# Optimization experiments

Measured on AMD Instinct MI355X. Metric: run time of the kernel, lower is better.

Reference implementation:

```python
import jax, jax.numpy as jnp
import numpy as np

B, N, S, K, D = 16, 4096, 1024, 32, 64
MLP = (64, 64, 128)
EPS = 1e-5  # BatchNorm2d default eps


def setup_inputs() -> dict:
    key = jax.random.key(0)
    ks = jax.random.split(key, 16)
    inp = {
        'xyz': jax.random.normal(ks[0], (B, N, 3), dtype=jnp.float32),
        'normals': jax.random.normal(ks[1], (B, N, 3), dtype=jnp.float32),
        'points': jax.random.normal(ks[2], (B, N, D), dtype=jnp.float32),
        'fps_idx': jax.random.randint(ks[3], (B, S), 0, N),
    }
    last = D
    for i, c in enumerate(MLP):
        inp[f'w{i}'] = jax.random.normal(ks[4 + i], (c, last), dtype=jnp.float32) * (1.0 / np.sqrt(last))
        inp[f'b{i}'] = jnp.zeros((c,), dtype=jnp.float32)
        inp[f'g{i}'] = jnp.ones((c,), dtype=jnp.float32)
        inp[f'bt{i}'] = jnp.zeros((c,), dtype=jnp.float32)
        last = c
    return inp


def _group(points, idx):
    # points: [B,N,C], idx: [B,S,K] -> [B,S,K,C]
    b, s, k = idx.shape
    flat = idx.reshape(b, s * k)
    g = jnp.take_along_axis(points, flat[:, :, None], axis=1)
    return g.reshape(b, s, k, points.shape[-1])


def _forward(xyz, normals, points, fps_idx, params):
    new_xyz = jnp.take_along_axis(xyz, fps_idx[:, :, None], axis=1)        # [B,S,3]
    new_normals = jnp.take_along_axis(normals, fps_idx[:, :, None], axis=1)
    # squared distances [B,S,N] (algebraic form of the broadcasted cdist)
    d = (jnp.sum(new_xyz ** 2, -1)[:, :, None]
         + jnp.sum(xyz ** 2, -1)[:, None, :]
         - 2.0 * jnp.einsum('bsc,bnc->bsn', new_xyz, xyz))
    _, idx = jax.lax.top_k(-d, K)                                          # K nearest
    x = _group(points, idx)                                                # [B,S,K,D]
    x = jnp.transpose(x, (0, 3, 2, 1))                                     # [B,D,K,S]
    for (w, b, g, bt) in params:
        x = jnp.einsum('oc,bcks->boks', w, x) + b[None, :, None, None]     # 1x1 conv
        m = jnp.mean(x, axis=(0, 2, 3), keepdims=True)                     # BN (batch stats)
        v = jnp.var(x, axis=(0, 2, 3), keepdims=True)
        x = (x - m) * jax.lax.rsqrt(v + EPS) * g[None, :, None, None] + bt[None, :, None, None]
        x = jax.nn.relu(x)
    feat = jnp.transpose(jnp.max(x, axis=2), (0, 2, 1))                    # [B,S,C_out]
    return new_xyz, new_normals, feat, fps_idx


def reference(xyz, normals, points, fps_idx,
              w0, b0, g0, bt0, w1, b1, g1, bt1, w2, b2, g2, bt2):
    params = ((w0, b0, g0, bt0), (w1, b1, g1, bt1), (w2, b2, g2, bt2))
    return _forward(xyz, normals, points, fps_idx, params)
```

## Files before the change

### kernel.cpp

```cpp
#include <hip/hip_runtime.h>
#include <hip/hip_bf16.h>

#define B_ 16
#define N_ 4096
#define S_ 1024
#define K_ 32
#define D_ 64
#define M_ (B_*S_*K_)
#define U_ (B_*N_)
#define EPS_ 1e-5f

#define OUT_NRM  (B_*S_*3)
#define OUT_FEAT (2*B_*S_*3)
#define OUT_FPS  (OUT_FEAT + B_*S_*128)

typedef __attribute__((ext_vector_type(8))) short bf16x8;
typedef __attribute__((ext_vector_type(4))) float f32x4;
typedef unsigned long long u64;

__device__ __forceinline__ unsigned short rnb(float x){
  return (unsigned short)((__float_as_uint(x) + 0x8000u) >> 16);
}
__device__ __forceinline__ void split1(float x, short& h, short& l){
  unsigned ux = __float_as_uint(x);
  unsigned uh = (ux + 0x8000u) & 0xFFFF0000u;
  h = (short)(uh >> 16);
  float lo = x - __uint_as_float(uh);
  l = (short)((__float_as_uint(lo) + 0x8000u) >> 16);
}
__device__ __forceinline__ unsigned f2key(float d){
  unsigned u = __float_as_uint(d);
  return u ^ ((unsigned)(((int)u) >> 31) | 0x80000000u);
}
__device__ __forceinline__ unsigned mprefix(u64 m){
  return __builtin_amdgcn_mbcnt_hi((unsigned)(m >> 32),
         __builtin_amdgcn_mbcnt_lo((unsigned)m, 0u));
}

__device__ __forceinline__ float hred4_sum(const float v[4], int l){
  bool hi8 = (l & 8) != 0;
  float send0 = hi8 ? v[0] : v[2];
  float send1 = hi8 ? v[1] : v[3];
  float r0 = __shfl_xor(send0, 8);
  float r1 = __shfl_xor(send1, 8);
  float a0 = (hi8 ? v[2] : v[0]) + r0;
  float a1 = (hi8 ? v[3] : v[1]) + r1;
  bool hi4 = (l & 4) != 0;
  float send = hi4 ? a0 : a1;
  float r = __shfl_xor(send, 4);
  float a = (hi4 ? a1 : a0) + r;
  a += __shfl_xor(a, 2);
  a += __shfl_xor(a, 1);
  return a;
}

__device__ __forceinline__ void bsort64_f32x2(float& v0, float& v1, int l){
  #pragma unroll
  for (int k = 2; k <= 64; k <<= 1){
    #pragma unroll
    for (int j = k >> 1; j > 0; j >>= 1){
      bool keepmn = (((l & k) == 0) == ((l & j) == 0));
      float o0 = __shfl_xor(v0, j);
      float o1 = __shfl_xor(v1, j);
      v0 = keepmn ? fminf(v0, o0) : fmaxf(v0, o0);
      v1 = keepmn ? fminf(v1, o1) : fmaxf(v1, o1);
    }
  }
}
__device__ __forceinline__ void bsort64_u64x2(u64& v0, u64& v1, int l){
  #pragma unroll
  for (int k = 2; k <= 64; k <<= 1){
    #pragma unroll
    for (int j = k >> 1; j > 0; j >>= 1){
      bool keepmn = (((l & k) == 0) == ((l & j) == 0));
      u64 o0 = __shfl_xor((unsigned long long)v0, j);
      u64 o1 = __shfl_xor((unsigned long long)v1, j);
      bool a0 = v0 < o0, a1 = v1 < o1;
      v0 = (a0 == keepmn) ? v0 : o0;
      v1 = (a1 == keepmn) ? v1 : o1;
    }
  }
}

__global__ void prep_kernel(const float* __restrict__ xyz, const float* __restrict__ nrm,
                            const int* __restrict__ fps,
                            const float* __restrict__ w0, const float* __restrict__ w1,
                            const float* __restrict__ w2,
                            float* __restrict__ out, float4* __restrict__ px,
                            unsigned short* __restrict__ wdst, float* __restrict__ stats,
                            unsigned* __restrict__ mult){
  const int bid = blockIdx.x, tid = threadIdx.x;
  if (bid < 256){
    int t = bid*256 + tid;
    const float* p = xyz + (size_t)t*3;
    float x = p[0], y = p[1], z = p[2];
    float pp = __fadd_rn(__fadd_rn(__fmul_rn(x,x), __fmul_rn(y,y)), __fmul_rn(z,z));
    px[t] = make_float4(__fmul_rn(-2.f,x), __fmul_rn(-2.f,y), __fmul_rn(-2.f,z), pp);
  } else if (bid < 320){
    int t = (bid-256)*256 + tid;
    int b = t >> 10;
    int n = fps[t];
    const float* xp = xyz + ((size_t)b*N_ + n)*3;
    out[t*3+0] = xp[0]; out[t*3+1] = xp[1]; out[t*3+2] = xp[2];
    const float* pp = nrm + ((size_t)b*N_ + n)*3;
    out[OUT_NRM + t*3+0] = pp[0]; out[OUT_NRM + t*3+1] = pp[1]; out[OUT_NRM + t*3+2] = pp[2];
    out[OUT_FPS + t] = (float)n;
  } else if (bid < 384){
    int e = (bid-320)*256 + tid;
    const float* W; int base;
    if (e < 4096){ W = w0; base = 0; }
    else if (e < 8192){ W = w1; base = 4096; }
    else { W = w2; base = 8192; }
    int r = e - base;
    int frag = r >> 9;
    int lane = (r >> 3) & 63;
    int j = r & 7;
    int cht = frag >> 1, ks = frag & 1;
    int m = lane & 15, quad = lane >> 4;
    int ch = cht*16 + m, k = ks*32 + quad*8 + j;
    wdst[e] = rnb(W[ch*64 + k]);
  } else if (bid < 400){
    stats[(bid-384)*256 + tid] = 0.f;
  } else {
    mult[(bid-400)*256 + tid] = 0u;
  }
}

#define DISTA(P,QX,QY,QZ,QQ) __builtin_fmaf((P).x,(QX), \
  __builtin_fmaf((P).y,(QY), __builtin_fmaf((P).z,(QZ), (P).w + (QQ))))

__device__ __forceinline__ float dist_exact(float4 P, float qx, float qy, float qz, float qq){
  float px = -0.5f*P.x, py = -0.5f*P.y, pz = -0.5f*P.z;
  float dt = __fadd_rn(__fadd_rn(__fmul_rn(qx,px), __fmul_rn(qy,py)), __fmul_rn(qz,pz));
  return __fsub_rn(__fadd_rn(qq,P.w), __fmul_rn(2.f,dt));
}

#define MARGIN_ 1e-3f

__device__ __forceinline__ void sel_fallback(const u64* sp, unsigned tot, int l,
                                             int* __restrict__ outp){
  if (tot <= 64){
    u64 pair = sp[l];
    u64 plo = 0, phi = (1ull << 44) - 1;
    for (int it = 0; it < 44; ++it){
      u64 mid = plo + ((phi - plo) >> 1);
      u64 m = __ballot(pair <= mid);
      if (__popcll(m) >= 32) phi = mid; else plo = mid + 1;
    }
    bool sel = (pair <= plo);
    u64 m = __ballot(sel);
    unsigned pos = mprefix(m);
    if (sel) outp[pos] = (int)(pair & 0xFFFull);
  } else {
    u64 pa = sp[l], pb = sp[64 + l];
    u64 plo = 0, phi = (1ull << 44) - 1;
    for (int it = 0; it < 44; ++it){
      u64 mid = plo + ((phi - plo) >> 1);
      int c = __popcll(__ballot(pa <= mid)) + __popcll(__ballot(pb <= mid));
      if (c >= 32) phi = mid; else plo = mid + 1;
    }
    int ca = (pa <= plo) ? 1 : 0;
    int cb = (pb <= plo) ? 1 : 0;
    int c2 = ca + cb, inc = c2;
    #pragma unroll
    for (int off = 1; off < 64; off <<= 1){
      int tv = __shfl_up(inc, off);
      if (l >= off) inc += tv;
    }
    int pos = inc - c2;
    if (ca){ outp[pos] = (int)(pa & 0xFFFull); pos++; }
    if (cb){ outp[pos] = (int)(pb & 0xFFFull); }
  }
}

__global__ __launch_bounds__(256, 8) void knn_kernel(const float4* __restrict__ pxyz,
                                                     const int* __restrict__ fps,
                                                     int* __restrict__ idxout){
  __shared__ u64 spair[4][2][128];
  const int t = threadIdx.x, w = t >> 6, l = t & 63;
  const int b = blockIdx.x >> 7;
  const float4* __restrict__ Pp = pxyz + (size_t)b*N_;
  const int q0 = blockIdx.x*8 + w*2;
  const int nq0 = fps[q0], nq1 = fps[q0+1];
  const float4 Q0 = Pp[nq0], Q1 = Pp[nq1];
  const float qx0 = -0.5f*Q0.x, qy0 = -0.5f*Q0.y, qz0 = -0.5f*Q0.z, qq0 = Q0.w;
  const float qx1 = -0.5f*Q1.x, qy1 = -0.5f*Q1.y, qz1 = -0.5f*Q1.z, qq1 = Q1.w;

  float vmin0 = 3.0e38f, vmin1 = 3.0e38f;
  #pragma unroll 8
  for (int i = 0; i < 64; i++){
    float4 P = Pp[i*64 + l];
    float d0 = DISTA(P, qx0, qy0, qz0, qq0); vmin0 = fminf(vmin0, d0);
    float d1 = DISTA(P, qx1, qy1, qz1, qq1); vmin1 = fminf(vmin1, d1);
  }

  float s0 = vmin0, s1 = vmin1;
  bsort64_f32x2(s0, s1, l);
  const float Tm0 = __shfl(s0, 31) + MARGIN_;
  const float Tm1 = __shfl(s1, 31) + MARGIN_;

  spair[w][0][l] = ~0ull; spair[w][0][64 + l] = ~0ull;
  spair[w][1][l] = ~0ull; spair[w][1][64 + l] = ~0ull;

  unsigned cnt0 = 0, cnt1 = 0;
  #pragma unroll 4
  for (int i = 0; i < 64; i++){
    unsigned n = (unsigned)(i*64 + l);
    float4 P = Pp[n];
    {
      float da = DISTA(P, qx0, qy0, qz0, qq0);
      bool c = (da <= Tm0);
      u64 m = __ballot(c);
      if (c){
        float de = dist_exact(P, qx0, qy0, qz0, qq0);
        unsigned pos = cnt0 + mprefix(m);
        if (pos < 128) spair[w][0][pos] = ((u64)f2key(de) << 12) | n;
      }
      cnt0 += (unsigned)__popcll(m);
    }
    {
      float da = DISTA(P, qx1, qy1, qz1, qq1);
      bool c = (da <= Tm1);
      u64 m = __ballot(c);
      if (c){
        float de = dist_exact(P, qx1, qy1, qz1, qq1);
        unsigned pos = cnt1 + mprefix(m);
        if (pos < 128) spair[w][1][pos] = ((u64)f2key(de) << 12) | n;
      }
      cnt1 += (unsigned)__popcll(m);
    }
  }

  const size_t obase = (size_t)q0 * K_;
  if (cnt0 <= 64 && cnt1 <= 64){
    u64 P0 = spair[w][0][l], P1 = spair[w][1][l];
    bsort64_u64x2(P0, P1, l);
    if (l < 32){
      idxout[obase + l]      = (int)(P0 & 0xFFFull);
      idxout[obase + K_ + l] = (int)(P1 & 0xFFFull);
    }
  } else {
    sel_fallback(&spair[w][0][0], cnt0, l, idxout + obase);
    sel_fallback(&spair[w][1][0], cnt1, l, idxout + obase + K_);
  }
}

__global__ void hist_kernel(const int* __restrict__ idx, unsigned* __restrict__ mult){
  int i = blockIdx.x*256 + threadIdx.x;
  int b = i >> 15;
  atomicAdd(&mult[b*4096 + idx[i]], 1u);
}

__global__ __launch_bounds__(256, 4) void conv1_mfma(const float* __restrict__ pts,
    const unsigned* __restrict__ mult, const unsigned short* __restrict__ wpk,
    const float* __restrict__ bias, unsigned short* __restrict__ Yo,
    float* __restrict__ stats){
  __shared__ float sred[4][128];
  __shared__ uint4 Wl4[512];
  const unsigned short* Wl = (const unsigned short*)Wl4;
  const int t = threadIdx.x, w = t>>6, l = t&63, quad = l>>4, lr = l&15;
  const int Rw = blockIdx.x*128 + w*32;
  Wl4[t] = ((const uint4*)wpk)[t];
  Wl4[256 + t] = ((const uint4*)wpk)[256 + t];
  f32x4 acc[4][2];
  #pragma unroll
  for (int c = 0; c < 4; c++)
    #pragma unroll
    for (int rt = 0; rt < 2; rt++)
      acc[c][rt] = (f32x4){0.f,0.f,0.f,0.f};
  float mf[2];
  mf[0] = (float)mult[Rw + lr];
  mf[1] = (float)mult[Rw + 16 + lr];
  __syncthreads();
  #pragma unroll
  for (int s = 0; s < 2; s++){
    bf16x8 wfs[4];
    #pragma unroll
    for (int c = 0; c < 4; c++)
      wfs[c] = *(const bf16x8*)(Wl + (((c*2+s)<<6) + l)*8);
    #pragma unroll
    for (int rt = 0; rt < 2; rt++){
      const float* pr = pts + (size_t)(Rw + rt*16 + lr)*64;
      float4 v0 = *(const float4*)(pr + s*32 + quad*8);
      float4 v1 = *(const float4*)(pr + s*32 + quad*8 + 4);
      float xs[8] = {v0.x,v0.y,v0.z,v0.w,v1.x,v1.y,v1.z,v1.w};
      bf16x8 xh, xl;
      #pragma unroll
      for (int j = 0; j < 8; j++){ short hh, ll; split1(xs[j], hh, ll); xh[j]=hh; xl[j]=ll; }
      #pragma unroll
      for (int c = 0; c < 4; c++){
        acc[c][rt] = __builtin_amdgcn_mfma_f32_16x16x32_bf16(wfs[c], xh, acc[c][rt], 0,0,0);
        acc[c][rt] = __builtin_amdgcn_mfma_f32_16x16x32_bf16(wfs[c], xl, acc[c][rt], 0,0,0);
      }
    }
  }
  const int rtg0 = Rw >> 4;
  #pragma unroll
  for (int c = 0; c < 4; c++){
    float4 bq = *(const float4*)(bias + c*16 + quad*4);
    float bqa[4] = {bq.x, bq.y, bq.z, bq.w};
    float sv[4] = {0,0,0,0}, qv[4] = {0,0,0,0};
    int kb = c*2 + (quad>>1);
    int sub = (quad&1)*4;
    #pragma unroll
    for (int rt = 0; rt < 2; rt++){
      float y[4];
      #pragma unroll
      for (int r = 0; r < 4; r++){
        y[r] = acc[c][rt][r] + bqa[r];
        sv[r] += mf[rt]*y[r];
        qv[r] += mf[rt]*y[r]*y[r];
      }
      uint2 p;
      p.x = (unsigned)rnb(y[0]) | ((unsigned)rnb(y[1])<<16);
      p.y = (unsigned)rnb(y[2]) | ((unsigned)rnb(y[3])<<16);
      *(uint2*)(Yo + ((((rtg0+rt)*8 + kb)*16 + lr)*8 + sub)) = p;
    }
    float S = hred4_sum(sv, l);
    float Q = hred4_sum(qv, l);
    if ((l & 3) == 0){
      int ch = c*16 + quad*4 + ((l>>3)&1)*2 + ((l>>2)&1);
      sred[w][ch] = S;
      sred[w][64 + ch] = Q;
    }
  }
  __syncthreads();
  if (t < 128){
    float tot = sred[0][t]+sred[1][t]+sred[2][t]+sred[3][t];
    unsafeAtomicAdd(&stats[(blockIdx.x & 7)*512 + t], tot);
  }
}

__global__ __launch_bounds__(256, 4) void conv2_mfma(const unsigned short* __restrict__ Yi,
    const unsigned* __restrict__ mult, const unsigned short* __restrict__ wpk,
    const float* __restrict__ bias, const float* __restrict__ gg,
    const float* __restrict__ btv, unsigned short* __restrict__ Yo,
    float* __restrict__ stats){
  __shared__ float sred[4][128];
  __shared__ float sAff[128];
  __shared__ uint4 Wl4[512];
  const unsigned short* Wl = (const unsigned short*)Wl4;
  const int t = threadIdx.x, w = t>>6, l = t&63, quad = l>>4, lr = l&15;
  const int Rw = blockIdx.x*128 + w*32;
  Wl4[t] = ((const uint4*)wpk)[t];
  Wl4[256 + t] = ((const uint4*)wpk)[256 + t];
  if (t < 64){
    const float inv = 1.f/(float)M_;
    float S = 0.f, Q = 0.f;
    #pragma unroll
    for (int r = 0; r < 8; r++){
      S += stats[r*512 + t];
      Q += stats[r*512 + 64 + t];
    }
    float mean = S * inv;
    float var  = Q * inv - mean*mean;
    float a = gg[t] * rsqrtf(var + EPS_);
    sAff[t] = a;
    sAff[64 + t] = btv[t] - mean*a;
  }
  f32x4 acc[4][2];
  #pragma unroll
  for (int c = 0; c < 4; c++)
    #pragma unroll
    for (int rt = 0; rt < 2; rt++)
      acc[c][rt] = (f32x4){0.f,0.f,0.f,0.f};
  float mf[2];
  mf[0] = (float)mult[Rw + lr];
  mf[1] = (float)mult[Rw + 16 + lr];
  const int rtg0 = Rw >> 4;
  uint4 u[2][2];
  #pragma unroll
  for (int s = 0; s < 2; s++)
    #pragma unroll
    for (int rt = 0; rt < 2; rt++)
      u[s][rt] = *(const uint4*)(Yi + (((rtg0+rt)*8 + s*4 + quad)*16 + lr)*8);
  __syncthreads();
  #pragma unroll
  for (int s = 0; s < 2; s++){
    float4 A0 = *(const float4*)(sAff + s*32 + quad*8);
    float4 A1 = *(const float4*)(sAff + s*32 + quad*8 + 4);
    float4 B0 = *(const float4*)(sAff + 64 + s*32 + quad*8);
    float4 B1 = *(const float4*)(sAff + 64 + s*32 + quad*8 + 4);
    float aA[8] = {A0.x,A0.y,A0.z,A0.w,A1.x,A1.y,A1.z,A1.w};
    float aB[8] = {B0.x,B0.y,B0.z,B0.w,B1.x,B1.y,B1.z,B1.w};
    bf16x8 wfs[4];
    #pragma unroll
    for (int c = 0; c < 4; c++)
      wfs[c] = *(const bf16x8*)(Wl + (((c*2+s)<<6) + l)*8);
    #pragma unroll
    for (int rt = 0; rt < 2; rt++){
      unsigned ua[4] = {u[s][rt].x, u[s][rt].y, u[s][rt].z, u[s][rt].w};
      bf16x8 xb;
      #pragma unroll
      for (int j = 0; j < 8; j++){
        unsigned wd = ua[j>>1];
        float yf = __uint_as_float((j&1) ? (wd & 0xFFFF0000u) : (wd << 16));
        float x = fmaxf(0.f, fmaf(yf, aA[j], aB[j]));
        xb[j] = (short)rnb(x);
      }
      #pragma unroll
      for (int c = 0; c < 4; c++)
        acc[c][rt] = __builtin_amdgcn_mfma_f32_16x16x32_bf16(wfs[c], xb, acc[c][rt], 0,0,0);
    }
  }
  #pragma unroll
  for (int c = 0; c < 4; c++){
    float4 bq = *(const float4*)(bias + c*16 + quad*4);
    float bqa[4] = {bq.x, bq.y, bq.z, bq.w};
    float sv[4] = {0,0,0,0}, qv[4] = {0,0,0,0};
    int kb = c*2 + (quad>>1);
    int sub = (quad&1)*4;
    #pragma unroll
    for (int rt = 0; rt < 2; rt++){
      float y[4];
      #pragma unroll
      for (int r = 0; r < 4; r++){
        y[r] = acc[c][rt][r] + bqa[r];
        sv[r] += mf[rt]*y[r];
        qv[r] += mf[rt]*y[r]*y[r];
      }
      uint2 p;
      p.x = (unsigned)rnb(y[0]) | ((unsigned)rnb(y[1])<<16);
      p.y = (unsigned)rnb(y[2]) | ((unsigned)rnb(y[3])<<16);
      *(uint2*)(Yo + ((((rtg0+rt)*8 + kb)*16 + lr)*8 + sub)) = p;
    }
    float S = hred4_sum(sv, l);
    float Q = hred4_sum(qv, l);
    if ((l & 3) == 0){
      int ch = c*16 + quad*4 + ((l>>3)&1)*2 + ((l>>2)&1);
      sred[w][ch] = S;
      sred[w][64 + ch] = Q;
    }
  }
  __syncthreads();
  if (t < 128){
    float tot = sred[0][t]+sred[1][t]+sred[2][t]+sred[3][t];
    unsafeAtomicAdd(&stats[(blockIdx.x & 7)*512 + 128 + t], tot);
  }
}

__global__ __launch_bounds__(256, 3) void conv3_mfma(const unsigned short* __restrict__ Yi,
    const unsigned* __restrict__ mult, const unsigned short* __restrict__ wpk,
    const float* __restrict__ bias, const float* __restrict__ gg,
    const float* __restrict__ btv, float* __restrict__ zout,
    float* __restrict__ stats){
  __shared__ float sred[4][256];
  __shared__ float sAff[128];
  __shared__ uint4 Wl4[1024];
  const unsigned short* Wl = (const unsigned short*)Wl4;
  const int t = threadIdx.x, w = t>>6, l = t&63, quad = l>>4, lr = l&15;
  const int Rw = blockIdx.x*128 + w*32;
  #pragma unroll
  for (int i = 0; i < 4; i++) Wl4[i*256 + t] = ((const uint4*)wpk)[i*256 + t];
  if (t < 64){
    const float inv = 1.f/(float)M_;
    float S = 0.f, Q = 0.f;
    #pragma unroll
    for (int r = 0; r < 8; r++){
      S += stats[r*512 + 128 + t];
      Q += stats[r*512 + 192 + t];
    }
    float mean = S * inv;
    float var  = Q * inv - mean*mean;
    float a = gg[t] * rsqrtf(var + EPS_);
    sAff[t] = a;
    sAff[64 + t] = btv[t] - mean*a;
  }
  f32x4 acc[8][2];
  #pragma unroll
  for (int c = 0; c < 8; c++){
    acc[c][0] = (f32x4){0.f,0.f,0.f,0.f};
    acc[c][1] = (f32x4){0.f,0.f,0.f,0.f};
  }
  float mf[2];
  mf[0] = (float)mult[Rw + lr];
  mf[1] = (float)mult[Rw + 16 + lr];
  const int rtg0 = Rw >> 4;
  uint4 u[2][2];
  #pragma unroll
  for (int s = 0; s < 2; s++)
    #pragma unroll
    for (int rt = 0; rt < 2; rt++)
      u[s][rt] = *(const uint4*)(Yi + (((rtg0+rt)*8 + s*4 + quad)*16 + lr)*8);
  __syncthreads();
  #pragma unroll
  for (int s = 0; s < 2; s++){
    float4 A0 = *(const float4*)(sAff + s*32 + quad*8);
    float4 A1 = *(const float4*)(sAff + s*32 + quad*8 + 4);
    float4 B0 = *(const float4*)(sAff + 64 + s*32 + quad*8);
    float4 B1 = *(const float4*)(sAff + 64 + s*32 + quad*8 + 4);
    float aA[8] = {A0.x,A0.y,A0.z,A0.w,A1.x,A1.y,A1.z,A1.w};
    float aB[8] = {B0.x,B0.y,B0.z,B0.w,B1.x,B1.y,B1.z,B1.w};
    #pragma unroll
    for (int rt = 0; rt < 2; rt++){
      unsigned ua[4] = {u[s][rt].x, u[s][rt].y, u[s][rt].z, u[s][rt].w};
      bf16x8 xb;
      #pragma unroll
      for (int j = 0; j < 8; j++){
        unsigned wd = ua[j>>1];
        float yf = __uint_as_float((j&1) ? (wd & 0xFFFF0000u) : (wd << 16));
        float x = fmaxf(0.f, fmaf(yf, aA[j], aB[j]));
        xb[j] = (short)rnb(x);
      }
      #pragma unroll
      for (int c = 0; c < 8; c++){
        bf16x8 wfc = *(const bf16x8*)(Wl + (((c*2+s)<<6) + l)*8);
        acc[c][rt] = __builtin_amdgcn_mfma_f32_16x16x32_bf16(wfc, xb, acc[c][rt], 0,0,0);
      }
    }
  }
  #pragma unroll
  for (int c = 0; c < 8; c++){
    float4 bq = *(const float4*)(bias + c*16 + quad*4);
    float bqa[4] = {bq.x, bq.y, bq.z, bq.w};
    float sv[4], qv[4];
    #pragma unroll
    for (int rt = 0; rt < 2; rt++){
      float y[4];
      #pragma unroll
      for (int r = 0; r < 4; r++){
        y[r] = acc[c][rt][r] + bqa[r];
        float wy = mf[rt]*y[r];
        if (rt == 0){ sv[r] = wy; qv[r] = wy*y[r]; }
        else        { sv[r] += wy; qv[r] += wy*y[r]; }
      }
      *(float4*)(zout + (size_t)(Rw + rt*16 + lr)*128 + c*16 + quad*4)
          = make_float4(y[0], y[1], y[2], y[3]);
    }
    float S = hred4_sum(sv, l);
    float Q = hred4_sum(qv, l);
    if ((l & 3) == 0){
      int ch = c*16 + quad*4 + ((l>>3)&1)*2 + ((l>>2)&1);
      sred[w][ch] = S;
      sred[w][128 + ch] = Q;
    }
  }
  __syncthreads();
  {
    float tot = sred[0][t]+sred[1][t]+sred[2][t]+sred[3][t];
    unsafeAtomicAdd(&stats[(blockIdx.x & 7)*512 + 256 + t], tot);
  }
}

__global__ __launch_bounds__(256, 8) void maxpool_kernel(const int* __restrict__ idx,
    const float* __restrict__ zout, float* __restrict__ ymax){
  __shared__ int sid[4][32];
  const int t = threadIdx.x, w = t>>6, l = t&63;
  const int q = blockIdx.x*4 + w;
  if (l < 32) sid[w][l] = idx[q*32 + l];
  __syncthreads();
  const float* zb = zout + (size_t)(q >> 10) * 4096 * 128;
  float mx = -3.4e38f, my = -3.4e38f;
  #pragma unroll 8
  for (int s = 0; s < 32; s++){
    const float* zp = zb + (size_t)sid[w][s]*128 + l*2;
    float vx = zp[0], vy = zp[1];
    mx = fmaxf(mx, vx);
    my = fmaxf(my, vy);
  }
  ymax[(size_t)q*128 + l*2]     = mx;
  ymax[(size_t)q*128 + l*2 + 1] = my;
}

__global__ void final_kernel(const float* __restrict__ ymax,
                             const float* __restrict__ stats,
                             const float* __restrict__ gg, const float* __restrict__ btv,
                             float* __restrict__ out){
  __shared__ float sA[128], sB[128];
  const int tid = threadIdx.x;
  if (tid < 128){
    const float inv = 1.f/(float)M_;
    float S = 0.f, Q = 0.f;
    #pragma unroll
    for (int r = 0; r < 8; r++){
      S += stats[r*512 + 256 + tid];
      Q += stats[r*512 + 384 + tid];
    }
    float mean = S * inv;
    float var  = Q * inv - mean*mean;
    float a = gg[tid] * rsqrtf(var + EPS_);
    sA[tid] = a;
    sB[tid] = btv[tid] - mean*a;
  }
  __syncthreads();
  const size_t base = ((size_t)blockIdx.x*256 + tid)*8;
  float4 v0 = *(const float4*)(ymax + base);
  float4 v1 = *(const float4*)(ymax + base + 4);
  const int c0 = (int)(base & 127);
  float4 a0 = *(const float4*)(sA + c0);
  float4 a1 = *(const float4*)(sA + c0 + 4);
  float4 b0 = *(const float4*)(sB + c0);
  float4 b1 = *(const float4*)(sB + c0 + 4);
  float4 o0, o1;
  o0.x = fmaxf(0.f, a0.x*v0.x + b0.x); o0.y = fmaxf(0.f, a0.y*v0.y + b0.y);
  o0.z = fmaxf(0.f, a0.z*v0.z + b0.z); o0.w = fmaxf(0.f, a0.w*v0.w + b0.w);
  o1.x = fmaxf(0.f, a1.x*v1.x + b1.x); o1.y = fmaxf(0.f, a1.y*v1.y + b1.y);
  o1.z = fmaxf(0.f, a1.z*v1.z + b1.z); o1.w = fmaxf(0.f, a1.w*v1.w + b1.w);
  *(float4*)(out + OUT_FEAT + base) = o0;
  *(float4*)(out + OUT_FEAT + base + 4) = o1;
}

extern "C" void kernel_launch(void* const* d_in, const int* in_sizes, int n_in,
                              void* d_out, int out_size, void* d_ws, size_t ws_size,
                              hipStream_t stream) {
  const float* xyz = (const float*)d_in[0];
  const float* nrm = (const float*)d_in[1];
  const float* pts = (const float*)d_in[2];
  const int*   fps = (const int*)d_in[3];
  const float* w0  = (const float*)d_in[4];
  const float* b0  = (const float*)d_in[5];
  const float* g0  = (const float*)d_in[6];
  const float* bt0 = (const float*)d_in[7];
  const float* w1  = (const float*)d_in[8];
  const float* b1  = (const float*)d_in[9];
  const float* g1  = (const float*)d_in[10];
  const float* bt1 = (const float*)d_in[11];
  const float* w2  = (const float*)d_in[12];
  const float* b2  = (const float*)d_in[13];
  const float* g2  = (const float*)d_in[14];
  const float* bt2 = (const float*)d_in[15];
  float* out = (float*)d_out;

  char* ws = (char*)d_ws;
  float* stats = (float*)ws;
  int*   idxb  = (int*)(ws + 20480);
  float* ymax  = (float*)(ws + 2117632);
  float4* pxyz = (float4*)(ws + 10506240);
  unsigned short* wpack = (unsigned short*)(ws + 11554816);
  unsigned* mult = (unsigned*)(ws + 11620352);
  unsigned short* Y1 = (unsigned short*)(ws + 16777216);
  unsigned short* Y2 = (unsigned short*)(ws + 33554432);
  float* zout = (float*)(ws + 50331648);

  prep_kernel<<<656, 256, 0, stream>>>(xyz, nrm, fps, w0, w1, w2, out, pxyz, wpack, stats, mult);
  knn_kernel<<<2048, 256, 0, stream>>>(pxyz, fps, idxb);
  hist_kernel<<<2048, 256, 0, stream>>>(idxb, mult);
  conv1_mfma<<<512, 256, 0, stream>>>(pts, mult, wpack, b0, Y1, stats);
  conv2_mfma<<<512, 256, 0, stream>>>(Y1, mult, wpack + 4096, b1, g0, bt0, Y2, stats);
  conv3_mfma<<<512, 256, 0, stream>>>(Y2, mult, wpack + 8192, b2, g1, bt1, zout, stats);
  maxpool_kernel<<<4096, 256, 0, stream>>>(idxb, zout, ymax);
  final_kernel<<<1024, 256, 0, stream>>>(ymax, stats, g2, bt2, out);
}
```

Before: 217.2 us.

## Fuse histogram into KNN kernel and BN/ReLU epilogue into maxpool

The KNN kernel now increments the per-batch multiplicity histogram with atomics at the moment it writes each neighbour index, which removes the separate hist kernel and its re-read of the index buffer. The maxpool kernel now computes the final BatchNorm scale and shift from the stats and applies BN+ReLU directly, which removes the ymax intermediate buffer and the final kernel launch. The cost is extra atomics inside KNN and a redundant stats reduction in each maxpool block.

```diff
diff --git a/kernel.cpp b/kernel.cpp
--- a/kernel.cpp
+++ b/kernel.cpp
@@ -138,7 +138,8 @@
 #define MARGIN_ 1e-3f
 
 __device__ __forceinline__ void sel_fallback(const u64* sp, unsigned tot, int l,
-                                             int* __restrict__ outp){
+                                             int* __restrict__ outp,
+                                             unsigned* __restrict__ multb){
   if (tot <= 64){
     u64 pair = sp[l];
     u64 plo = 0, phi = (1ull << 44) - 1;
@@ -150,7 +151,11 @@
     bool sel = (pair <= plo);
     u64 m = __ballot(sel);
     unsigned pos = mprefix(m);
-    if (sel) outp[pos] = (int)(pair & 0xFFFull);
+    if (sel){
+      int iv = (int)(pair & 0xFFFull);
+      outp[pos] = iv;
+      atomicAdd(&multb[iv], 1u);
+    }
   } else {
     u64 pa = sp[l], pb = sp[64 + l];
     u64 plo = 0, phi = (1ull << 44) - 1;
@@ -168,18 +173,29 @@
       if (l >= off) inc += tv;
     }
     int pos = inc - c2;
-    if (ca){ outp[pos] = (int)(pa & 0xFFFull); pos++; }
-    if (cb){ outp[pos] = (int)(pb & 0xFFFull); }
+    if (ca){
+      int iv = (int)(pa & 0xFFFull);
+      outp[pos] = iv;
+      atomicAdd(&multb[iv], 1u);
+      pos++;
+    }
+    if (cb){
+      int iv = (int)(pb & 0xFFFull);
+      outp[pos] = iv;
+      atomicAdd(&multb[iv], 1u);
+    }
   }
 }
 
 __global__ __launch_bounds__(256, 8) void knn_kernel(const float4* __restrict__ pxyz,
                                                      const int* __restrict__ fps,
-                                                     int* __restrict__ idxout){
+                                                     int* __restrict__ idxout,
+                                                     unsigned* __restrict__ mult){
   __shared__ u64 spair[4][2][128];
   const int t = threadIdx.x, w = t >> 6, l = t & 63;
   const int b = blockIdx.x >> 7;
   const float4* __restrict__ Pp = pxyz + (size_t)b*N_;
+  unsigned* __restrict__ multb = mult + (size_t)b*N_;
   const int q0 = blockIdx.x*8 + w*2;
   const int nq0 = fps[q0], nq1 = fps[q0+1];
   const float4 Q0 = Pp[nq0], Q1 = Pp[nq1];
@@ -236,19 +252,17 @@
     u64 P0 = spair[w][0][l], P1 = spair[w][1][l];
     bsort64_u64x2(P0, P1, l);
     if (l < 32){
-      idxout[obase + l]      = (int)(P0 & 0xFFFull);
-      idxout[obase + K_ + l] = (int)(P1 & 0xFFFull);
+      int i0 = (int)(P0 & 0xFFFull);
+      int i1 = (int)(P1 & 0xFFFull);
+      idxout[obase + l]      = i0;
+      idxout[obase + K_ + l] = i1;
+      atomicAdd(&multb[i0], 1u);
+      atomicAdd(&multb[i1], 1u);
     }
   } else {
-    sel_fallback(&spair[w][0][0], cnt0, l, idxout + obase);
-    sel_fallback(&spair[w][1][0], cnt1, l, idxout + obase + K_);
-  }
-}
-
-__global__ void hist_kernel(const int* __restrict__ idx, unsigned* __restrict__ mult){
-  int i = blockIdx.x*256 + threadIdx.x;
-  int b = i >> 15;
-  atomicAdd(&mult[b*4096 + idx[i]], 1u);
+    sel_fallback(&spair[w][0][0], cnt0, l, idxout + obase, multb);
+    sel_fallback(&spair[w][1][0], cnt1, l, idxout + obase + K_, multb);
+  }
 }
 
 __global__ __launch_bounds__(256, 4) void conv1_mfma(const float* __restrict__ pts,
@@ -542,12 +556,29 @@
   }
 }
 
-__global__ __launch_bounds__(256, 8) void maxpool_kernel(const int* __restrict__ idx,
-    const float* __restrict__ zout, float* __restrict__ ymax){
+__global__ __launch_bounds__(256, 8) void maxpool_final(const int* __restrict__ idx,
+    const float* __restrict__ zout, const float* __restrict__ stats,
+    const float* __restrict__ gg, const float* __restrict__ btv,
+    float* __restrict__ out){
   __shared__ int sid[4][32];
+  __shared__ float sA[128], sB[128];
   const int t = threadIdx.x, w = t>>6, l = t&63;
   const int q = blockIdx.x*4 + w;
   if (l < 32) sid[w][l] = idx[q*32 + l];
+  if (t < 128){
+    const float inv = 1.f/(float)M_;
+    float S = 0.f, Q = 0.f;
+    #pragma unroll
+    for (int r = 0; r < 8; r++){
+      S += stats[r*512 + 256 + t];
+      Q += stats[r*512 + 384 + t];
+    }
+    float mean = S * inv;
+    float var  = Q * inv - mean*mean;
+    float a = gg[t] * rsqrtf(var + EPS_);
+    sA[t] = a;
+    sB[t] = btv[t] - mean*a;
+  }
   __syncthreads();
   const float* zb = zout + (size_t)(q >> 10) * 4096 * 128;
   float mx = -3.4e38f, my = -3.4e38f;
@@ -558,46 +589,9 @@
     mx = fmaxf(mx, vx);
     my = fmaxf(my, vy);
   }
-  ymax[(size_t)q*128 + l*2]     = mx;
-  ymax[(size_t)q*128 + l*2 + 1] = my;
-}
-
-__global__ void final_kernel(const float* __restrict__ ymax,
-                             const float* __restrict__ stats,
-                             const float* __restrict__ gg, const float* __restrict__ btv,
-                             float* __restrict__ out){
-  __shared__ float sA[128], sB[128];
-  const int tid = threadIdx.x;
-  if (tid < 128){
-    const float inv = 1.f/(float)M_;
-    float S = 0.f, Q = 0.f;
-    #pragma unroll
-    for (int r = 0; r < 8; r++){
-      S += stats[r*512 + 256 + tid];
-      Q += stats[r*512 + 384 + tid];
-    }
-    float mean = S * inv;
-    float var  = Q * inv - mean*mean;
-    float a = gg[tid] * rsqrtf(var + EPS_);
-    sA[tid] = a;
-    sB[tid] = btv[tid] - mean*a;
-  }
-  __syncthreads();
-  const size_t base = ((size_t)blockIdx.x*256 + tid)*8;
-  float4 v0 = *(const float4*)(ymax + base);
-  float4 v1 = *(const float4*)(ymax + base + 4);
-  const int c0 = (int)(base & 127);
-  float4 a0 = *(const float4*)(sA + c0);
-  float4 a1 = *(const float4*)(sA + c0 + 4);
-  float4 b0 = *(const float4*)(sB + c0);
-  float4 b1 = *(const float4*)(sB + c0 + 4);
-  float4 o0, o1;
-  o0.x = fmaxf(0.f, a0.x*v0.x + b0.x); o0.y = fmaxf(0.f, a0.y*v0.y + b0.y);
-  o0.z = fmaxf(0.f, a0.z*v0.z + b0.z); o0.w = fmaxf(0.f, a0.w*v0.w + b0.w);
-  o1.x = fmaxf(0.f, a1.x*v1.x + b1.x); o1.y = fmaxf(0.f, a1.y*v1.y + b1.y);
-  o1.z = fmaxf(0.f, a1.z*v1.z + b1.z); o1.w = fmaxf(0.f, a1.w*v1.w + b1.w);
-  *(float4*)(out + OUT_FEAT + base) = o0;
-  *(float4*)(out + OUT_FEAT + base + 4) = o1;
+  const int c0 = l*2, c1 = l*2 + 1;
+  out[OUT_FEAT + (size_t)q*128 + c0] = fmaxf(0.f, sA[c0]*mx + sB[c0]);
+  out[OUT_FEAT + (size_t)q*128 + c1] = fmaxf(0.f, sA[c1]*my + sB[c1]);
 }
 
 extern "C" void kernel_launch(void* const* d_in, const int* in_sizes, int n_in,
@@ -624,7 +618,6 @@
   char* ws = (char*)d_ws;
   float* stats = (float*)ws;
   int*   idxb  = (int*)(ws + 20480);
-  float* ymax  = (float*)(ws + 2117632);
   float4* pxyz = (float4*)(ws + 10506240);
   unsigned short* wpack = (unsigned short*)(ws + 11554816);
   unsigned* mult = (unsigned*)(ws + 11620352);
@@ -633,11 +626,9 @@
   float* zout = (float*)(ws + 50331648);
 
   prep_kernel<<<656, 256, 0, stream>>>(xyz, nrm, fps, w0, w1, w2, out, pxyz, wpack, stats, mult);
-  knn_kernel<<<2048, 256, 0, stream>>>(pxyz, fps, idxb);
-  hist_kernel<<<2048, 256, 0, stream>>>(idxb, mult);
+  knn_kernel<<<2048, 256, 0, stream>>>(pxyz, fps, idxb, mult);
   conv1_mfma<<<512, 256, 0, stream>>>(pts, mult, wpack, b0, Y1, stats);
   conv2_mfma<<<512, 256, 0, stream>>>(Y1, mult, wpack + 4096, b1, g0, bt0, Y2, stats);
   conv3_mfma<<<512, 256, 0, stream>>>(Y2, mult, wpack + 8192, b2, g1, bt1, zout, stats);
-  maxpool_kernel<<<4096, 256, 0, stream>>>(idxb, zout, ymax);
-  final_kernel<<<1024, 256, 0, stream>>>(ymax, stats, g2, bt2, out);
-}
+  maxpool_final<<<4096, 256, 0, stream>>>(idxb, zout, stats, g2, bt2, out);
+}
```

Result: faster. 201.9 us, median of 2 (-7.1%).
